# Kernel tuning notes

Hardware: AMD Instinct MI355X
Metric: run time of the kernel (lower is better)

The kernel has to match this reference:

```python
import jax, jax.numpy as jnp
import numpy as np

N_NODES = 50000
N_EDGES = 400000
N_GRAPHS = 512
F = 32        # num_features
NB = 32       # mp_num_basis_fn
ZMAX = 118
CUTOFF = 5.0
NSPH = 9      # (mp_max_degree+1)^2 with max_degree=2
DEG_IDX = jnp.array([0, 1, 1, 1, 2, 2, 2, 2, 2])  # degree of each spherical component


def _bernstein(u, n=NB):
    # reciprocal_bernstein radial basis: Bernstein polynomials of degree n-1 at u in [0,1)
    k = jnp.arange(n, dtype=jnp.float32)
    log_binom = (jax.scipy.special.gammaln(float(n)) - jax.scipy.special.gammaln(k + 1.0)
                 - jax.scipy.special.gammaln(float(n) - k))
    u = jnp.clip(u, 1e-7, 1.0 - 1e-7)[..., None]
    return jnp.exp(log_binom + k * jnp.log(u) + (float(n) - 1.0 - k) * jnp.log1p(-u))


def _smooth_cutoff(r, cutoff=CUTOFF):
    t = r / cutoff
    return jnp.where(t < 1.0, jnp.exp(1.0 - 1.0 / jnp.clip(1.0 - t * t, 1e-7, None)), 0.0)


def _sph(u):
    # real spherical harmonics (cartesian normalization) up to degree 2; u: (E,3) unit vectors
    x, y, z = u[:, 0], u[:, 1], u[:, 2]
    c = jnp.sqrt(jnp.float32(3.0))
    return jnp.stack([jnp.ones_like(x), y, z, x,
                      c * x * y, c * y * z, 0.5 * (3.0 * z * z - 1.0),
                      c * z * x, 0.5 * c * (x * x - y * y)], axis=-1)


def _dense(x, W, b):
    # equivariant Dense: shared kernel over spherical components, bias only on scalar (l=0)
    y = jnp.einsum('nmf,fg->nmg', x, W)
    return y.at[:, 0, :].add(b)


def _silu_gate(x):
    # equivariant silu: scalar channel gates all degrees (scalar part -> exact silu)
    return x * jax.nn.sigmoid(x[:, 0:1, :])


def setup_inputs() -> dict:
    key = jax.random.key(0)
    ks = jax.random.split(key, 24)
    s = 1.0 / np.sqrt(F)
    sb = 1.0 / np.sqrt(NB)
    inp = {
        'positions': 2.0 * jax.random.normal(ks[0], (N_NODES, 3), jnp.float32),
        'embed': jax.random.normal(ks[1], (ZMAX, F), jnp.float32),
        'Wy0': sb * jax.random.normal(ks[2], (3, NB, F), jnp.float32),
        'Wx0': sb * jax.random.normal(ks[3], (3, NB, F), jnp.float32),
        'W1_0': s * jax.random.normal(ks[4], (F, F), jnp.float32),
        'b1_0': jnp.zeros((F,), jnp.float32),
        'W2_0': s * jax.random.normal(ks[5], (F, F), jnp.float32),
        'b2_0': jnp.zeros((F,), jnp.float32),
        'c0': jnp.full((1,), 0.5, jnp.float32),
        'Wr_last': sb * jax.random.normal(ks[6], (NB, F), jnp.float32),
        'W1_1': s * jax.random.normal(ks[7], (F, F), jnp.float32),
        'b1_1': jnp.zeros((F,), jnp.float32),
        'W2_1': s * jax.random.normal(ks[8], (F, F), jnp.float32),
        'b2_1': jnp.zeros((F,), jnp.float32),
        'c1': jnp.full((1,), 0.5, jnp.float32),
        'Wro1': s * jax.random.normal(ks[9], (F, F), jnp.float32),
        'bro1': jnp.zeros((F,), jnp.float32),
        'Wro2': s * jax.random.normal(ks[10], (F, 1), jnp.float32),
        'bro2': jnp.zeros((1,), jnp.float32),
        'atomic_bias': jax.random.normal(ks[11], (ZMAX,), jnp.float32),
        'atomic_numbers': jax.random.randint(ks[12], (N_NODES,), 0, ZMAX, jnp.int32),
        'dst_idx': jax.random.randint(ks[13], (N_EDGES,), 0, N_NODES, jnp.int32),
        'src_idx': jax.random.randint(ks[14], (N_EDGES,), 0, N_NODES, jnp.int32),
        'batch_segments': jnp.sort(jax.random.randint(ks[15], (N_NODES,), 0, N_GRAPHS, jnp.int32)),
        'graph_mask': jnp.ones((N_GRAPHS,), jnp.bool_),
    }
    return inp


def reference(positions, embed, Wy0, Wx0, W1_0, b1_0, W2_0, b2_0, c0,
              Wr_last, W1_1, b1_1, W2_1, b2_1, c1,
              Wro1, bro1, Wro2, bro2, atomic_bias,
              atomic_numbers, dst_idx, src_idx, batch_segments, graph_mask):
    # --- edge geometry (gather_src/gather_dst) ---
    disp = positions[src_idx] - positions[dst_idx]                # (E,3)
    r = jnp.sqrt(jnp.sum(disp * disp, axis=-1) + 1e-12)           # (E,)
    u = disp / r[:, None]
    Y = _sph(u)                                                   # (E,9)
    rbf = _bernstein(r / (r + 1.0)) * _smooth_cutoff(r)[:, None]  # (E,NB)

    # --- atomic embedding, lifted to (N, 9, F) with zero higher degrees ---
    x0 = embed[atomic_numbers]                                    # (N,F)
    x = jnp.concatenate([x0[:, None, :], jnp.zeros((N_NODES, NSPH - 1, F), x0.dtype)], axis=1)

    # --- iteration 0: full-degree equivariant message pass ---
    wy = jnp.einsum('eb,lbf->elf', rbf, Wy0)[:, DEG_IDX, :]       # (E,9,F) radial weights, (0,l)->l path
    wx = jnp.einsum('eb,lbf->elf', rbf, Wx0)[:, DEG_IDX, :]       # (l,0)->l path
    xs = x[src_idx]                                               # (E,9,F)
    msg = wy * Y[:, :, None] * xs[:, 0:1, :] + wx * xs
    y = jax.ops.segment_sum(msg, dst_idx, num_segments=N_NODES)   # (N,9,F)
    y = x + y
    y = _silu_gate(_dense(y, W1_0, b1_0))
    y = _dense(y, W2_0, b2_0)
    x = x + jax.nn.silu(c0) * y                                   # y_nl == 0 (era disabled)

    # --- iteration 1 (last): max_degree=0 message pass, then reduce to scalars ---
    w0 = rbf @ Wr_last                                            # (E,F)
    msg0 = w0 * x[src_idx, 0, :]
    y0 = jax.ops.segment_sum(msg0, dst_idx, num_segments=N_NODES) # (N,F)
    xs0 = x[:, 0, :]                                              # change_max_degree -> scalars
    y0 = xs0 + y0
    y0 = jax.nn.silu(y0 @ W1_1 + b1_1)
    y0 = y0 @ W2_1 + b2_1
    xs0 = xs0 + jax.nn.silu(c1) * y0

    # --- atomic readout and per-graph sum ---
    h = jax.nn.silu(xs0 @ Wro1 + bro1)
    e_atom = (h @ Wro2)[:, 0] + bro2[0] + atomic_bias[atomic_numbers]
    e_graph = jax.ops.segment_sum(e_atom, batch_segments, num_segments=N_GRAPHS)
    return jnp.where(graph_mask, e_graph, 0.0)
```

## Files before the change

### kernel.cpp

```cpp
#include <hip/hip_runtime.h>
#include <math.h>

#define NNODES 50000
#define NEDGES 400000
#define NGRAPHS 512
#define FDIM 32
#define CAP 32

#define NHALVES 4096
#define NQ   (NNODES / NHALVES)
#define NREM (NNODES % NHALVES)

static constexpr float BINOM31[32] = {
    1.f, 31.f, 465.f, 4495.f, 31465.f, 169911.f, 736281.f, 2629575.f,
    7888725.f, 20160075.f, 44352165.f, 84672315.f, 141120525.f, 206253075.f,
    265182525.f, 300540195.f, 300540195.f, 265182525.f, 206253075.f,
    141120525.f, 84672315.f, 44352165.f, 20160075.f, 7888725.f, 2629575.f,
    736281.f, 169911.f, 31465.f, 4495.f, 465.f, 31.f, 1.f
};

__device__ __forceinline__ float fast_rcp(float x) {
    return __builtin_amdgcn_rcpf(x);
}
__device__ __forceinline__ float silu(float x) {
    return x * fast_rcp(1.0f + __expf(-x));
}

__global__ __launch_bounds__(256) void build_csr(
    const float* __restrict__ pos,
    const int* __restrict__ srci, const int* __restrict__ dsti,
    const int* __restrict__ Z,
    float4* __restrict__ pay, int* __restrict__ deg)
{
    int e = blockIdx.x * 256 + threadIdx.x;
    if (e >= NEDGES) return;
    int s = srci[e], d = dsti[e];
    float dx = pos[3 * s]     - pos[3 * d];
    float dy = pos[3 * s + 1] - pos[3 * d + 1];
    float dz = pos[3 * s + 2] - pos[3 * d + 2];
    float r = sqrtf(dx * dx + dy * dy + dz * dz + 1e-12f);
    if (r >= 5.0f) return;

    float t = r * 0.2f;
    float q = fmaxf(1.0f - t * t, 1e-7f);
    float cut = __expf(1.0f - fast_rcp(q));
    float v = fast_rcp(r + 1.0f);
    float v2 = v * v, v4 = v2 * v2, v8 = v4 * v4, v16 = v8 * v8;
    float scale = v16 * v8 * v4 * v2 * v * cut;

    int rank = atomicAdd(&deg[d], 1);
    if (rank < CAP)
        pay[(size_t)d * CAP + rank] =
            make_float4(r, scale,
                        __int_as_float(s * FDIM),
                        __int_as_float(Z[s] * FDIM));
}

#define GATHER_REG(ACC, XSRC, ROWSEL)                                      \
    float ACC = 0.0f;                                                      \
    if (dgr > 0) {                                                         \
        const float4* slot = pay + (size_t)n * CAP;                        \
        float4 _pa = h0c, _pb = h1c;                                       \
        for (int j = 0; ; j += 2) {                                        \
            float _xa = (XSRC)[__float_as_int(_pa.ROWSEL) + f];            \
            float _xb = (XSRC)[__float_as_int(_pb.ROWSEL) + f];            \
            float4 _na = slot[j + 2];                                      \
            float4 _nb = slot[j + 3];                                      \
            float _r2a = _pa.x * _pa.x, _r2b = _pb.x * _pb.x;              \
            float _ea = cw[30], _oa = cw[31];                              \
            float _eb = cw[30], _ob = cw[31];                              \
            _Pragma("unroll")                                              \
            for (int p = 14; p >= 0; --p) {                                \
                _ea = fmaf(_ea, _r2a, cw[2 * p]);                          \
                _oa = fmaf(_oa, _r2a, cw[2 * p + 1]);                      \
                _eb = fmaf(_eb, _r2b, cw[2 * p]);                          \
                _ob = fmaf(_ob, _r2b, cw[2 * p + 1]);                      \
            }                                                              \
            float _wa = fmaf(_pa.x, _oa, _ea);                             \
            float _wb = fmaf(_pb.x, _ob, _eb);                             \
            ACC = fmaf(_pa.y * _wa, _xa, ACC);                             \
            ACC = fmaf(_pb.y * _wb, _xb, ACC);                             \
            if (j + 2 >= dgr) break;                                       \
            _pa = _na; _pb = _nb;                                          \
        }                                                                  \
    }

#define MATVEC32R(RES, WR, BIAS) do {                                      \
    float4 _q0=yp[0], _q1=yp[1], _q2=yp[2], _q3=yp[3];                     \
    float4 _q4=yp[4], _q5=yp[5], _q6=yp[6], _q7=yp[7];                     \
    float _a0=(BIAS), _a1=0.f, _a2=0.f, _a3=0.f;                           \
    _a0=fmaf(_q0.x,WR[ 0],_a0); _a0=fmaf(_q0.y,WR[ 1],_a0);                \
    _a0=fmaf(_q0.z,WR[ 2],_a0); _a0=fmaf(_q0.w,WR[ 3],_a0);                \
    _a1=fmaf(_q1.x,WR[ 4],_a1); _a1=fmaf(_q1.y,WR[ 5],_a1);                \
    _a1=fmaf(_q1.z,WR[ 6],_a1); _a1=fmaf(_q1.w,WR[ 7],_a1);                \
    _a2=fmaf(_q2.x,WR[ 8],_a2); _a2=fmaf(_q2.y,WR[ 9],_a2);                \
    _a2=fmaf(_q2.z,WR[10],_a2); _a2=fmaf(_q2.w,WR[11],_a2);                \
    _a3=fmaf(_q3.x,WR[12],_a3); _a3=fmaf(_q3.y,WR[13],_a3);                \
    _a3=fmaf(_q3.z,WR[14],_a3); _a3=fmaf(_q3.w,WR[15],_a3);                \
    _a0=fmaf(_q4.x,WR[16],_a0); _a0=fmaf(_q4.y,WR[17],_a0);                \
    _a0=fmaf(_q4.z,WR[18],_a0); _a0=fmaf(_q4.w,WR[19],_a0);                \
    _a1=fmaf(_q5.x,WR[20],_a1); _a1=fmaf(_q5.y,WR[21],_a1);                \
    _a1=fmaf(_q5.z,WR[22],_a1); _a1=fmaf(_q5.w,WR[23],_a1);                \
    _a2=fmaf(_q6.x,WR[24],_a2); _a2=fmaf(_q6.y,WR[25],_a2);                \
    _a2=fmaf(_q6.z,WR[26],_a2); _a2=fmaf(_q6.w,WR[27],_a2);                \
    _a3=fmaf(_q7.x,WR[28],_a3); _a3=fmaf(_q7.y,WR[29],_a3);                \
    _a3=fmaf(_q7.z,WR[30],_a3); _a3=fmaf(_q7.w,WR[31],_a3);                \
    RES = (_a0+_a1)+(_a2+_a3); } while (0)

__device__ __forceinline__ void half_range(int h, int& n0, int& n1) {
    int a = h < NREM ? h * (NQ + 1) : NREM * (NQ + 1) + (h - NREM) * NQ;
    n0 = a;
    n1 = a + (h < NREM ? NQ + 1 : NQ);
}

__global__ __launch_bounds__(256, 2) void fused_a(
    const float4* __restrict__ pay, const int* __restrict__ deg,
    const float* __restrict__ embed, const int* __restrict__ Z,
    const float* __restrict__ Wy0, const float* __restrict__ Wx0,
    const float* __restrict__ W1, const float* __restrict__ b1,
    const float* __restrict__ W2, const float* __restrict__ b2,
    const float* __restrict__ c0,
    float* __restrict__ x1buf)
{
    __shared__ __align__(16) float ylds[4][64];
    int tid = threadIdx.x;
    int widx = tid >> 6;
    int lane = tid & 63;
    int f    = lane & 31;
    int half = lane >> 5;

    float cw[32], w1r[32], w2r[32];
    #pragma unroll
    for (int k = 0; k < 32; ++k) {
        cw[k]  = BINOM31[k] * (Wy0[k * FDIM + f] + Wx0[k * FDIM + f]);
        w1r[k] = W1[k * FDIM + f];
        w2r[k] = W2[k * FDIM + f];
    }
    float b1f = b1[f], b2f = b2[f];
    float sc0 = silu(c0[0]);

    int hidx = (blockIdx.x * 4 + widx) * 2 + half;
    int n0, n1;
    half_range(hidx, n0, n1);

    float* yrow = &ylds[widx][half * 32];
    const float4* yp = (const float4*)yrow;

    int dgr = min(deg[n0], CAP);
    const float4* sl0 = pay + (size_t)n0 * CAP;
    float4 h0c = sl0[0], h1c = sl0[1];
    float x0 = embed[Z[n0] * FDIM + f];

    for (int n = n0; n < n1; ++n) {
        GATHER_REG(accv, embed, w)

        int nn = (n + 1 < n1) ? n + 1 : n;
        int dgr_n = min(deg[nn], CAP);
        const float4* sln = pay + (size_t)nn * CAP;
        float4 h0n = sln[0], h1n = sln[1];
        float x0n = embed[Z[nn] * FDIM + f];

        yrow[f] = x0 + accv;
        float t;
        MATVEC32R(t, w1r, b1f);
        t = silu(t);
        yrow[f] = t;
        float u;
        MATVEC32R(u, w2r, b2f);
        x1buf[(size_t)n * FDIM + f] = fmaf(sc0, u, x0);

        dgr = dgr_n; h0c = h0n; h1c = h1n; x0 = x0n;
    }
}

__global__ __launch_bounds__(256, 2) void fused_b(
    const float4* __restrict__ pay, const int* __restrict__ deg,
    const float* __restrict__ x1buf, const float* __restrict__ Wr_last,
    const float* __restrict__ W1, const float* __restrict__ b1,
    const float* __restrict__ W2, const float* __restrict__ b2,
    const float* __restrict__ c1,
    const float* __restrict__ Wro1, const float* __restrict__ bro1,
    const float* __restrict__ Wro2, const float* __restrict__ bro2,
    const float* __restrict__ abias, const int* __restrict__ Z,
    const int* __restrict__ segs,
    float* __restrict__ out)
{
    __shared__ __align__(16) float ylds[4][64];
    int tid = threadIdx.x;
    int widx = tid >> 6;
    int lane = tid & 63;
    int f    = lane & 31;
    int half = lane >> 5;

    float cw[32], w1r[32], w2r[32], wrr[32];
    #pragma unroll
    for (int k = 0; k < 32; ++k) {
        cw[k]  = BINOM31[k] * Wr_last[k * FDIM + f];
        w1r[k] = W1[k * FDIM + f];
        w2r[k] = W2[k * FDIM + f];
        wrr[k] = Wro1[k * FDIM + f];
    }
    float b1f = b1[f], b2f = b2[f], bro1f = bro1[f], wro2f = Wro2[f];
    float sc1 = silu(c1[0]);
    float bro2v = bro2[0];

    int hidx = (blockIdx.x * 4 + widx) * 2 + half;
    int n0, n1;
    half_range(hidx, n0, n1);

    float* yrow = &ylds[widx][half * 32];
    const float4* yp = (const float4*)yrow;

    int dgr = min(deg[n0], CAP);
    const float4* sl0 = pay + (size_t)n0 * CAP;
    float4 h0c = sl0[0], h1c = sl0[1];
    float x1 = x1buf[(size_t)n0 * FDIM + f];
    float ab = abias[Z[n0]];
    int   sg = segs[n0];

    float segacc = 0.0f;
    int   curseg = -1;

    for (int n = n0; n < n1; ++n) {
        GATHER_REG(accv, x1buf, z)

        int nn = (n + 1 < n1) ? n + 1 : n;
        int dgr_n = min(deg[nn], CAP);
        const float4* sln = pay + (size_t)nn * CAP;
        float4 h0n = sln[0], h1n = sln[1];
        float x1n = x1buf[(size_t)nn * FDIM + f];
        float abn = abias[Z[nn]];
        int   sgn = segs[nn];

        yrow[f] = x1 + accv;
        float t;
        MATVEC32R(t, w1r, b1f);
        t = silu(t);
        yrow[f] = t;
        float u;
        MATVEC32R(u, w2r, b2f);
        float xs0 = fmaf(sc1, u, x1);
        yrow[f] = xs0;
        float h;
        MATVEC32R(h, wrr, bro1f);
        float p = silu(h) * wro2f;
        p += __shfl_xor(p, 16, 32);
        p += __shfl_xor(p, 8, 32);
        p += __shfl_xor(p, 4, 32);
        p += __shfl_xor(p, 2, 32);
        p += __shfl_xor(p, 1, 32);

        if (f == 0) {
            float e = p + bro2v + ab;
            if (sg == curseg) segacc += e;
            else {
                if (curseg >= 0) atomicAdd(&out[curseg], segacc);
                curseg = sg; segacc = e;
            }
        }

        dgr = dgr_n; h0c = h0n; h1c = h1n; x1 = x1n; ab = abn; sg = sgn;
    }
    if (f == 0 && curseg >= 0) atomicAdd(&out[curseg], segacc);
}

extern "C" void kernel_launch(void* const* d_in, const int* in_sizes, int n_in,
                              void* d_out, int out_size, void* d_ws, size_t ws_size,
                              hipStream_t stream)
{
    const float* pos     = (const float*)d_in[0];
    const float* embed   = (const float*)d_in[1];
    const float* Wy0     = (const float*)d_in[2];
    const float* Wx0     = (const float*)d_in[3];
    const float* W1_0    = (const float*)d_in[4];
    const float* b1_0    = (const float*)d_in[5];
    const float* W2_0    = (const float*)d_in[6];
    const float* b2_0    = (const float*)d_in[7];
    const float* c0      = (const float*)d_in[8];
    const float* Wr_last = (const float*)d_in[9];
    const float* W1_1    = (const float*)d_in[10];
    const float* b1_1    = (const float*)d_in[11];
    const float* W2_1    = (const float*)d_in[12];
    const float* b2_1    = (const float*)d_in[13];
    const float* c1      = (const float*)d_in[14];
    const float* Wro1    = (const float*)d_in[15];
    const float* bro1    = (const float*)d_in[16];
    const float* Wro2    = (const float*)d_in[17];
    const float* bro2    = (const float*)d_in[18];
    const float* abias   = (const float*)d_in[19];
    const int*   Z       = (const int*)d_in[20];
    const int*   dsti    = (const int*)d_in[21];
    const int*   srci    = (const int*)d_in[22];
    const int*   segs    = (const int*)d_in[23];

    float* out = (float*)d_out;

    char* w = (char*)d_ws;
    float4* pay   = (float4*)w;  w += (size_t)NNODES * CAP * 16;
    float*  x1buf = (float*)w;   w += (size_t)NNODES * FDIM * 4;
    int*    deg   = (int*)w;     w += (size_t)NNODES * 4;

    const int edgeBlocks = (NEDGES + 255) / 256;
    const int persBlocks = NHALVES / 8;

    hipMemsetAsync(pay, 0, (size_t)NNODES * CAP * 16, stream);
    hipMemsetAsync(deg, 0, (size_t)NNODES * 4, stream);
    hipMemsetAsync(out, 0, (size_t)NGRAPHS * 4, stream);

    build_csr<<<edgeBlocks, 256, 0, stream>>>(pos, srci, dsti, Z, pay, deg);
    fused_a<<<persBlocks, 256, 0, stream>>>(pay, deg, embed, Z, Wy0, Wx0,
                                            W1_0, b1_0, W2_0, b2_0, c0, x1buf);
    fused_b<<<persBlocks, 256, 0, stream>>>(pay, deg, x1buf, Wr_last,
                                            W1_1, b1_1, W2_1, b2_1, c1,
                                            Wro1, bro1, Wro2, bro2,
                                            abias, Z, segs, out);
}
```

Before: 189.2 us.

## Stage per-node edge payload in LDS and batch edges eight at a time

Each half-wave now loads a node's whole 32-slot edge payload with one coalesced per-lane load into LDS, prefetching the next node's payload during the current node's work. The old paired-edge loop with serial slot loads is replaced by processing edges in groups of 8. Each group gathers its features first, then evaluates the radial polynomial as a single 31-step Horner in r, giving 8 independent chains for more ILP. In exchange, degrees are padded up to a multiple of 8, so padding slots are computed and their gather indices are read. This relies on unused payload slots being zero-filled, and it wastes work on low-degree nodes.

```diff
diff --git a/kernel.cpp b/kernel.cpp
--- a/kernel.cpp
+++ b/kernel.cpp
@@ -56,33 +56,27 @@
                         __int_as_float(Z[s] * FDIM));
 }
 
-#define GATHER_REG(ACC, XSRC, ROWSEL)                                      \
+#define GATHER8(ACC, XSRC, SEL)                                            \
     float ACC = 0.0f;                                                      \
-    if (dgr > 0) {                                                         \
-        const float4* slot = pay + (size_t)n * CAP;                        \
-        float4 _pa = h0c, _pb = h1c;                                       \
-        for (int j = 0; ; j += 2) {                                        \
-            float _xa = (XSRC)[__float_as_int(_pa.ROWSEL) + f];            \
-            float _xb = (XSRC)[__float_as_int(_pb.ROWSEL) + f];            \
-            float4 _na = slot[j + 2];                                      \
-            float4 _nb = slot[j + 3];                                      \
-            float _r2a = _pa.x * _pa.x, _r2b = _pb.x * _pb.x;              \
-            float _ea = cw[30], _oa = cw[31];                              \
-            float _eb = cw[30], _ob = cw[31];                              \
+    for (int j = 0; j < dgc; j += 8) {                                     \
+        float rr[8], sc[8], xg[8], hh[8];                                  \
+        _Pragma("unroll")                                                  \
+        for (int k = 0; k < 8; ++k) {                                      \
+            float4 _p = pl[j + k];                                         \
+            rr[k] = _p.x; sc[k] = _p.y;                                    \
+            xg[k] = (XSRC)[__float_as_int(_p.SEL) + f];                    \
+        }                                                                  \
+        _Pragma("unroll")                                                  \
+        for (int k = 0; k < 8; ++k) hh[k] = cw[31];                        \
+        _Pragma("unroll")                                                  \
+        for (int t = 30; t >= 0; --t) {                                    \
             _Pragma("unroll")                                              \
-            for (int p = 14; p >= 0; --p) {                                \
-                _ea = fmaf(_ea, _r2a, cw[2 * p]);                          \
-                _oa = fmaf(_oa, _r2a, cw[2 * p + 1]);                      \
-                _eb = fmaf(_eb, _r2b, cw[2 * p]);                          \
-                _ob = fmaf(_ob, _r2b, cw[2 * p + 1]);                      \
-            }                                                              \
-            float _wa = fmaf(_pa.x, _oa, _ea);                             \
-            float _wb = fmaf(_pb.x, _ob, _eb);                             \
-            ACC = fmaf(_pa.y * _wa, _xa, ACC);                             \
-            ACC = fmaf(_pb.y * _wb, _xb, ACC);                             \
-            if (j + 2 >= dgr) break;                                       \
-            _pa = _na; _pb = _nb;                                          \
+            for (int k = 0; k < 8; ++k)                                    \
+                hh[k] = fmaf(hh[k], rr[k], cw[t]);                         \
         }                                                                  \
+        _Pragma("unroll")                                                  \
+        for (int k = 0; k < 8; ++k)                                        \
+            ACC = fmaf(sc[k] * hh[k], xg[k], ACC);                         \
     }
 
 #define MATVEC32R(RES, WR, BIAS) do {                                      \
@@ -123,6 +117,7 @@
     float* __restrict__ x1buf)
 {
     __shared__ __align__(16) float ylds[4][64];
+    __shared__ __align__(16) float4 plds[4][2][CAP];
     int tid = threadIdx.x;
     int widx = tid >> 6;
     int lane = tid & 63;
@@ -145,20 +140,24 @@
 
     float* yrow = &ylds[widx][half * 32];
     const float4* yp = (const float4*)yrow;
-
-    int dgr = min(deg[n0], CAP);
-    const float4* sl0 = pay + (size_t)n0 * CAP;
-    float4 h0c = sl0[0], h1c = sl0[1];
-    float x0 = embed[Z[n0] * FDIM + f];
+    float4* pl = &plds[widx][half][0];
+
+    float4 pv0 = pay[(size_t)n0 * CAP + f];
+    int dgc = min(deg[n0], CAP);
+    int zc  = Z[n0];
+    pl[f] = pv0;
+    float x0 = embed[zc * FDIM + f];
 
     for (int n = n0; n < n1; ++n) {
-        GATHER_REG(accv, embed, w)
-
         int nn = (n + 1 < n1) ? n + 1 : n;
-        int dgr_n = min(deg[nn], CAP);
-        const float4* sln = pay + (size_t)nn * CAP;
-        float4 h0n = sln[0], h1n = sln[1];
-        float x0n = embed[Z[nn] * FDIM + f];
+        float4 pvn = pay[(size_t)nn * CAP + f];
+        int dgn = min(deg[nn], CAP);
+        int zn  = Z[nn];
+
+        GATHER8(accv, embed, w)
+
+        float x0n = embed[zn * FDIM + f];
+        pl[f] = pvn;
 
         yrow[f] = x0 + accv;
         float t;
@@ -169,7 +168,7 @@
         MATVEC32R(u, w2r, b2f);
         x1buf[(size_t)n * FDIM + f] = fmaf(sc0, u, x0);
 
-        dgr = dgr_n; h0c = h0n; h1c = h1n; x0 = x0n;
+        dgc = dgn; x0 = x0n; zc = zn;
     }
 }
 
@@ -186,6 +185,7 @@
     float* __restrict__ out)
 {
     __shared__ __align__(16) float ylds[4][64];
+    __shared__ __align__(16) float4 plds[4][2][CAP];
     int tid = threadIdx.x;
     int widx = tid >> 6;
     int lane = tid & 63;
@@ -210,27 +210,31 @@
 
     float* yrow = &ylds[widx][half * 32];
     const float4* yp = (const float4*)yrow;
-
-    int dgr = min(deg[n0], CAP);
-    const float4* sl0 = pay + (size_t)n0 * CAP;
-    float4 h0c = sl0[0], h1c = sl0[1];
+    float4* pl = &plds[widx][half][0];
+
+    float4 pv0 = pay[(size_t)n0 * CAP + f];
+    int dgc = min(deg[n0], CAP);
+    int zc  = Z[n0];
+    int sg  = segs[n0];
+    pl[f] = pv0;
     float x1 = x1buf[(size_t)n0 * FDIM + f];
-    float ab = abias[Z[n0]];
-    int   sg = segs[n0];
+    float ab = abias[zc];
 
     float segacc = 0.0f;
     int   curseg = -1;
 
     for (int n = n0; n < n1; ++n) {
-        GATHER_REG(accv, x1buf, z)
-
         int nn = (n + 1 < n1) ? n + 1 : n;
-        int dgr_n = min(deg[nn], CAP);
-        const float4* sln = pay + (size_t)nn * CAP;
-        float4 h0n = sln[0], h1n = sln[1];
+        float4 pvn = pay[(size_t)nn * CAP + f];
+        int dgn = min(deg[nn], CAP);
+        int zn  = Z[nn];
+        int sgn = segs[nn];
+
+        GATHER8(accv, x1buf, z)
+
         float x1n = x1buf[(size_t)nn * FDIM + f];
-        float abn = abias[Z[nn]];
-        int   sgn = segs[nn];
+        float abn = abias[zn];
+        pl[f] = pvn;
 
         yrow[f] = x1 + accv;
         float t;
@@ -259,7 +263,7 @@
             }
         }
 
-        dgr = dgr_n; h0c = h0n; h1c = h1n; x1 = x1n; ab = abn; sg = sgn;
+        dgc = dgn; x1 = x1n; ab = abn; sg = sgn; zc = zn;
     }
     if (f == 0 && curseg >= 0) atomicAdd(&out[curseg], segacc);
 }
```

Result: faster. 185.0 us (-2.2%).
